# Kernel tuning notes

Measured on AMD Instinct MI355X. Metric: run time of the kernel, lower is better.

## Reference

```python
import jax, jax.numpy as jnp
import numpy as np

B, S, D, H = 2, 2048, 1024, 16
DK = D // H


def layernorm(x, gamma, bias, eps=1e-6):
    m = jnp.mean(x, axis=-1, keepdims=True)
    v = jnp.mean((x - m) ** 2, axis=-1, keepdims=True)  # biased var (correction=0)
    return gamma * (x - m) / jnp.sqrt(v + eps) + bias


def setup_inputs() -> dict:
    key = jax.random.key(0)
    ks = jax.random.split(key, 10)
    xav = (2.0 / (D + D)) ** 0.5  # xavier_normal_ std for square [D,D]
    lin1_b = (1.0 / D) ** 0.5     # nn.Linear default init bound
    lin2_b = (1.0 / (4 * D)) ** 0.5
    return {
        "X": jax.random.normal(ks[0], (B, S, D), jnp.float32),
        "padding_mask": jnp.ones((B, 1, S), jnp.int32),
        "W_Q": jax.random.normal(ks[1], (D, D), jnp.float32) * xav,
        "W_K": jax.random.normal(ks[2], (D, D), jnp.float32) * xav,
        "W_V": jax.random.normal(ks[3], (D, D), jnp.float32) * xav,
        "W_O": jax.random.normal(ks[4], (D, D), jnp.float32) * xav,
        "g1": jnp.ones((D,), jnp.float32),
        "b1": jnp.zeros((D,), jnp.float32),
        "W1": jax.random.uniform(ks[5], (D, 4 * D), jnp.float32, -lin1_b, lin1_b),
        "bias1": jax.random.uniform(ks[6], (4 * D,), jnp.float32, -lin1_b, lin1_b),
        "W2": jax.random.uniform(ks[7], (4 * D, D), jnp.float32, -lin2_b, lin2_b),
        "bias2": jax.random.uniform(ks[8], (D,), jnp.float32, -lin2_b, lin2_b),
        "g2": jnp.ones((D,), jnp.float32),
        "b2": jnp.zeros((D,), jnp.float32),
    }


def reference(X, padding_mask, W_Q, W_K, W_V, W_O, g1, b1, W1, bias1, W2, bias2, g2, b2):
    b, s, d = X.shape
    # pre-norm + MHA
    xn = layernorm(X, g1, b1)
    q = (xn @ W_Q).reshape(b, s, H, DK).transpose(0, 2, 1, 3)  # [B,H,S,DK]
    k = (xn @ W_K).reshape(b, s, H, DK).transpose(0, 2, 1, 3)
    v = (xn @ W_V).reshape(b, s, H, DK).transpose(0, 2, 1, 3)
    scores = jnp.einsum("bhqd,bhkd->bhqk", q, k) / np.sqrt(DK).astype(np.float32)
    mask = padding_mask[:, None, :, :]  # [B,1,1,S] broadcast over heads/queries
    scores = jnp.where(mask == 0, jnp.float32(-1e9), scores)
    w = jax.nn.softmax(scores, axis=-1)
    attn = jnp.einsum("bhqk,bhkd->bhqd", w, v)
    attn = attn.transpose(0, 2, 1, 3).reshape(b, s, d) @ W_O
    out = attn + X
    # pre-norm + GELU FFN (exact erf GELU, matching nn.GELU default)
    nn2 = layernorm(out, g2, b2)
    ff = jax.nn.gelu(nn2 @ W1 + bias1, approximate=False) @ W2 + bias2
    return ff + out
```

## Files before the change

### kernel.cpp

```cpp
#include <hip/hip_runtime.h>
#include <hip/hip_bf16.h>


using bf16 = __hip_bfloat16;
typedef __attribute__((ext_vector_type(4))) float f32x4;
typedef __attribute__((ext_vector_type(16))) float f32x16;
typedef __attribute__((ext_vector_type(8))) short bf16x8;

#define DEVI static __device__ __forceinline__

DEVI void async_copy16(const void* g, void* l) {
  __builtin_amdgcn_global_load_lds(
      (const __attribute__((address_space(1))) void*)g,
      (__attribute__((address_space(3))) void*)l, 16, 0, 0);
}

DEVI ushort f2bf_bits(float v) {
  __hip_bfloat16 h = __float2bfloat16(v);
  return *reinterpret_cast<ushort*>(&h);
}

DEVI float bfbits2f(ushort u) {
  union { float f; unsigned int i; } x;
  x.i = ((unsigned int)u) << 16;
  return x.f;
}

DEVI unsigned int pk2(float lo, float hi) {
  return (unsigned int)f2bf_bits(lo) | ((unsigned int)f2bf_bits(hi) << 16);
}

__global__ __launch_bounds__(256) void ln_kernel(
    const float* __restrict__ in, const float* __restrict__ gamma,
    const float* __restrict__ beta, bf16* __restrict__ out) {
  const long row = blockIdx.x;
  const int t = threadIdx.x;
  float4 x = ((const float4*)(in + row * 1024))[t];
  float s = x.x + x.y + x.z + x.w;
  float s2 = x.x * x.x + x.y * x.y + x.z * x.z + x.w * x.w;
#pragma unroll
  for (int m = 1; m < 64; m <<= 1) {
    s += __shfl_xor(s, m);
    s2 += __shfl_xor(s2, m);
  }
  __shared__ float red[8];
  const int w = t >> 6, l = t & 63;
  if (l == 0) { red[w] = s; red[4 + w] = s2; }
  __syncthreads();
  s = red[0] + red[1] + red[2] + red[3];
  s2 = red[4] + red[5] + red[6] + red[7];
  const float mean = s * (1.0f / 1024.0f);
  const float var = s2 * (1.0f / 1024.0f) - mean * mean;
  const float rstd = rsqrtf(var + 1e-6f);
  float4 g4 = ((const float4*)gamma)[t];
  float4 b4 = ((const float4*)beta)[t];
  union { ushort h[4]; uint2 u; } o;
  o.h[0] = f2bf_bits(g4.x * (x.x - mean) * rstd + b4.x);
  o.h[1] = f2bf_bits(g4.y * (x.y - mean) * rstd + b4.y);
  o.h[2] = f2bf_bits(g4.z * (x.z - mean) * rstd + b4.z);
  o.h[3] = f2bf_bits(g4.w * (x.w - mean) * rstd + b4.w);
  ((uint2*)(out + row * 1024))[t] = o.u;
}

__global__ __launch_bounds__(256) void oproj_reduce_ln(
    const float* __restrict__ p0, const float* __restrict__ p1,
    const float* __restrict__ X, const float* __restrict__ gamma,
    const float* __restrict__ beta, float* __restrict__ res_out,
    bf16* __restrict__ xn_out) {
  const long row = blockIdx.x;
  const int t = threadIdx.x;
  const long i = row * 256 + t;
  const float4 a = ((const float4*)p0)[i];
  const float4 b = ((const float4*)p1)[i];
  const float4 c = ((const float4*)X)[i];
  float4 x;
  x.x = a.x + b.x + c.x; x.y = a.y + b.y + c.y;
  x.z = a.z + b.z + c.z; x.w = a.w + b.w + c.w;
  ((float4*)res_out)[i] = x;
  float s = x.x + x.y + x.z + x.w;
  float s2 = x.x * x.x + x.y * x.y + x.z * x.z + x.w * x.w;
#pragma unroll
  for (int m = 1; m < 64; m <<= 1) {
    s += __shfl_xor(s, m);
    s2 += __shfl_xor(s2, m);
  }
  __shared__ float red[8];
  const int w = t >> 6, l = t & 63;
  if (l == 0) { red[w] = s; red[4 + w] = s2; }
  __syncthreads();
  s = red[0] + red[1] + red[2] + red[3];
  s2 = red[4] + red[5] + red[6] + red[7];
  const float mean = s * (1.0f / 1024.0f);
  const float var = s2 * (1.0f / 1024.0f) - mean * mean;
  const float rstd = rsqrtf(var + 1e-6f);
  float4 g4 = ((const float4*)gamma)[t];
  float4 b4 = ((const float4*)beta)[t];
  union { ushort h[4]; uint2 u; } o;
  o.h[0] = f2bf_bits(g4.x * (x.x - mean) * rstd + b4.x);
  o.h[1] = f2bf_bits(g4.y * (x.y - mean) * rstd + b4.y);
  o.h[2] = f2bf_bits(g4.z * (x.z - mean) * rstd + b4.z);
  o.h[3] = f2bf_bits(g4.w * (x.w - mean) * rstd + b4.w);
  ((uint2*)(xn_out + row * 1024))[t] = o.u;
}

__global__ __launch_bounds__(256) void transpose_all(
    const float* __restrict__ q, const float* __restrict__ k,
    const float* __restrict__ v, const float* __restrict__ o,
    const float* __restrict__ w1, const float* __restrict__ w2,
    bf16* __restrict__ wqkvo, bf16* __restrict__ w1t, bf16* __restrict__ w2t) {
  const int tid = blockIdx.x;
  const float* W;
  bf16* Wt;
  int K, N, n0, k0;
  if (tid < 4096) {
    const int z = tid >> 10, r = tid & 1023;
    W = (z == 0) ? q : (z == 1) ? k : (z == 2) ? v : o;
    Wt = wqkvo + (size_t)z * 1024 * 1024;
    K = 1024; N = 1024; n0 = (r & 31) << 5; k0 = (r >> 5) << 5;
  } else if (tid < 8192) {
    const int r = tid - 4096;
    W = w1; Wt = w1t; K = 1024; N = 4096;
    n0 = (r & 127) << 5; k0 = (r >> 7) << 5;
  } else {
    const int r = tid - 8192;
    W = w2; Wt = w2t; K = 4096; N = 1024;
    n0 = (r & 31) << 5; k0 = (r >> 5) << 5;
  }
  __shared__ float tile[32][33];
  const int tx = threadIdx.x & 31, ty = threadIdx.x >> 5;
#pragma unroll
  for (int i = 0; i < 32; i += 8)
    tile[ty + i][tx] = W[(long)(k0 + ty + i) * N + n0 + tx];
  __syncthreads();
#pragma unroll
  for (int i = 0; i < 32; i += 8)
    Wt[(long)(n0 + ty + i) * K + k0 + tx] = __float2bfloat16(tile[tx][ty + i]);
}

template <int EPI, int KSPLIT>
__global__ __launch_bounds__(256) void gemm_bt(
    const bf16* __restrict__ A, const bf16* __restrict__ Bt,
    const int M, const int N, const int K, const int lda, const int ldb,
    const float* __restrict__ bias, const float* __restrict__ res,
    float* __restrict__ pother, void* __restrict__ Cout) {
  __shared__ bf16 As[128 * 64];
  __shared__ bf16 Bs[128 * 64];
  const int t = threadIdx.x;
  const int w = t >> 6, l = t & 63;
  const int nb = N >> 7;
  const int cpx = gridDim.x >> 3;
  int bidx = (blockIdx.x & 7) * cpx + (blockIdx.x >> 3);
  int sl = 0;
  if (KSPLIT == 2) {
    const int half = gridDim.x >> 1;
    sl = bidx >= half;
    bidx -= sl * half;
  }
  const int bm = bidx / nb, bn = bidx % nb;
  const long row0 = (long)bm << 7, col0 = (long)bn << 7;
  const int wr = (w >> 1) << 6, wc = (w & 1) << 6;
  const int lr = l & 15;
  const int lkb = (l >> 4) << 4;

  f32x4 acc[4][4];
#pragma unroll
  for (int m = 0; m < 4; ++m)
#pragma unroll
    for (int n = 0; n < 4; ++n) acc[m][n] = (f32x4){0.f, 0.f, 0.f, 0.f};

  const int rA = t >> 3;
  const int g = (t & 7) ^ ((t >> 3) & 7);
  const bf16* gA = A + (row0 + rA) * (long)lda + (long)sl * K + g * 8;
  const bf16* gB = Bt + (col0 + rA) * (long)ldb + (long)sl * K + g * 8;
  char* lA = (char*)As + t * 16;
  char* lB = (char*)Bs + t * 16;

  for (int k0 = 0; k0 < K; k0 += 64) {
    __syncthreads();
#pragma unroll
    for (int cr = 0; cr < 4; ++cr) {
      async_copy16(gA + (long)cr * 32 * lda + k0, lA + cr * 4096);
      async_copy16(gB + (long)cr * 32 * ldb + k0, lB + cr * 4096);
    }
    __syncthreads();
#pragma unroll
    for (int ks = 0; ks < 2; ++ks) {
      bf16x8 af[4], bfr[4];
#pragma unroll
      for (int m = 0; m < 4; ++m) {
        const int row = wr + m * 16 + lr;
        af[m] = *(const bf16x8*)((const char*)As +
            (row * 128 + ((ks * 64 + lkb) ^ ((row & 7) << 4))));
      }
#pragma unroll
      for (int n = 0; n < 4; ++n) {
        const int row = wc + n * 16 + lr;
        bfr[n] = *(const bf16x8*)((const char*)Bs +
            (row * 128 + ((ks * 64 + lkb) ^ ((row & 7) << 4))));
      }
#pragma unroll
      for (int m = 0; m < 4; ++m)
#pragma unroll
        for (int n = 0; n < 4; ++n)
          acc[m][n] = __builtin_amdgcn_mfma_f32_16x16x32_bf16(af[m], bfr[n], acc[m][n], 0, 0, 0);
    }
  }

  bf16* Cb = (bf16*)Cout;
  float* Cf = (float*)Cout;
  if ((EPI == 4 || EPI == 5) && sl == 1) Cf = pother;
#pragma unroll
  for (int m = 0; m < 4; ++m) {
#pragma unroll
    for (int r = 0; r < 4; ++r) {
      const long crow = row0 + wr + m * 16 + ((l >> 4) << 2) + r;
      const long rbase = crow * N;
#pragma unroll
      for (int n = 0; n < 4; ++n) {
        const long ccol = col0 + wc + n * 16 + lr;
        float v = acc[m][n][r];
        if (EPI == 2) {
          const float vv = v + bias[ccol];
          const float u2 = vv * (1.5957691216f + 0.0713548162f * vv * vv);
          v = vv / (1.0f + __expf(-u2));
        }
        if (EPI == 5 && sl == 0) v += bias[ccol] + res[rbase + ccol];
        if (EPI == 0 || EPI == 2)
          Cb[rbase + ccol] = __float2bfloat16(v);
        else
          Cf[rbase + ccol] = v;
      }
    }
  }
}

__global__ __launch_bounds__(256) void ff2_reduce(
    const float* __restrict__ p0, const float* __restrict__ p1,
    float* __restrict__ out) {
  const int idx = blockIdx.x * 256 + threadIdx.x;
  const float4 x = ((const float4*)p0)[idx];
  const float4 y = ((const float4*)p1)[idx];
  float4 a;
  a.x = x.x + y.x; a.y = x.y + y.y; a.z = x.z + y.z; a.w = x.w + y.w;
  ((float4*)out)[idx] = a;
}

__global__ __launch_bounds__(512) void attn_kernel(
    const bf16* __restrict__ QKV, const int* __restrict__ pmask,
    bf16* __restrict__ Oout) {
  const int bh = blockIdx.x;
  const int b = bh >> 4, h = bh & 15;
  const int q0 = blockIdx.y << 8;
  const int t = threadIdx.x;
  const int w = t >> 6, l = t & 63;
  const int lq = l & 31, hi = l >> 5;

  __shared__ __align__(16) char smem[65536];

  const long base = (long)b * 2048 * 3072;
  const bf16* Qg = QKV + base + h * 64;
  const bf16* Kg = QKV + base + 1024 + h * 64;
  const bf16* Vg = QKV + base + 2048 + h * 64;

  int kSrc[2], kDst[2], vk[2], vsg[2];
#pragma unroll
  for (int p = 0; p < 2; ++p) {
    const int c = p * 512 + t;
    const int kr = c >> 3;
    kSrc[p] = kr * 3072 + (((c & 7) ^ (kr & 7)) << 3);
    kDst[p] = c * 16;
    vk[p] = c >> 3;
    vsg[p] = c & 7;
  }

  const int qw0 = q0 + w * 32;
  bf16x8 qf[4];
#pragma unroll
  for (int dc = 0; dc < 4; ++dc) {
    uint4 raw = *(const uint4*)(Qg + (long)(qw0 + lq) * 3072 + dc * 16 + hi * 8);
    union { uint4 u4; ushort us[8]; } in; in.u4 = raw;
    union { bf16x8 v; ushort us[8]; } o;
#pragma unroll
    for (int e = 0; e < 8; ++e) o.us[e] = f2bf_bits(0.125f * bfbits2f(in.us[e]));
    qf[dc] = o.v;
  }

  union { unsigned int u[4]; bf16x8 v; } bones;
  bones.u[0] = (hi == 0) ? 0x00003F80u : 0u;
  bones.u[1] = bones.u[2] = bones.u[3] = 0u;

  uint4 vreg[2];
#pragma unroll
  for (int p = 0; p < 2; ++p) {
    vreg[p] = *(const uint4*)(Vg + (long)vk[p] * 3072 + vsg[p] * 8);
    async_copy16(Kg + kSrc[p], smem + kDst[p]);
  }
#pragma unroll
  for (int p = 0; p < 2; ++p) {
    const ushort* vs = (const ushort*)&vreg[p];
#pragma unroll
    for (int e = 0; e < 8; ++e) {
      const int d = vsg[p] * 8 + e;
      *(ushort*)(smem + 32768 + d * 256 +
                 ((vk[p] * 2) ^ (((e ^ vsg[p]) & 7) << 4))) = vs[e];
    }
  }

  f32x16 oacc[2];
#pragma unroll
  for (int nt = 0; nt < 2; ++nt)
#pragma unroll
    for (int r = 0; r < 16; ++r) oacc[nt][r] = 0.f;
  float mrun = -3.0e38f, lsum = 0.f;
  int cur = 0;

  __syncthreads();

  for (int ktg = 0; ktg < 16; ++ktg) {
    if (ktg < 15) {
      const long nrow0 = (long)(ktg + 1) * 128 * 3072;
#pragma unroll
      for (int p = 0; p < 2; ++p) {
        vreg[p] = *(const uint4*)(Vg + nrow0 + (long)vk[p] * 3072 + vsg[p] * 8);
        async_copy16(Kg + nrow0 + kSrc[p], smem + (cur ^ 1) * 16384 + kDst[p]);
      }
    }
    const int k0 = ktg << 7;
    const char* Ks = smem + cur * 16384;
    const char* Vt = smem + 32768 + cur * 16384;

    f32x16 sacc[4];
    __builtin_amdgcn_s_setprio(1);
#pragma unroll
    for (int kt = 0; kt < 4; ++kt) {
#pragma unroll
      for (int r = 0; r < 16; ++r) sacc[kt][r] = 0.f;
#pragma unroll
      for (int dc = 0; dc < 4; ++dc) {
        bf16x8 ka = *(const bf16x8*)(Ks +
            ((kt * 32 + lq) * 128 + ((dc * 32 + hi * 16) ^ ((lq & 7) << 4))));
        sacc[kt] = __builtin_amdgcn_mfma_f32_32x32x16_bf16(ka, qf[dc], sacc[kt], 0, 0, 0);
      }
      const int mv = pmask[b * 2048 + k0 + kt * 32 + lq];
      union { unsigned int u[4]; bf16x8 v; } aadd;
      aadd.u[0] = (hi == 0 && mv == 0) ? (unsigned int)f2bf_bits(-1.0e9f) : 0u;
      aadd.u[1] = aadd.u[2] = aadd.u[3] = 0u;
      sacc[kt] = __builtin_amdgcn_mfma_f32_32x32x16_bf16(aadd.v, bones.v, sacc[kt], 0, 0, 0);
    }
    __builtin_amdgcn_s_setprio(0);

    float tmax = -3.0e38f;
#pragma unroll
    for (int kt = 0; kt < 4; ++kt)
#pragma unroll
      for (int r = 0; r < 16; ++r) tmax = fmaxf(tmax, sacc[kt][r]);
    tmax = fmaxf(tmax, __shfl_xor(tmax, 32));
    const bool need = (bool)__any(tmax > mrun + 8.0f);
    const float mnew = need ? fmaxf(mrun, tmax) : mrun;
    float psum = 0.f;
#pragma unroll
    for (int kt = 0; kt < 4; ++kt)
#pragma unroll
      for (int r = 0; r < 16; ++r) {
        const float p = __expf(sacc[kt][r] - mnew);
        sacc[kt][r] = p;
        psum += p;
      }
    psum += __shfl_xor(psum, 32);
    if (need) {
      const float alpha = __expf(mrun - mnew);
      mrun = mnew;
      lsum = lsum * alpha + psum;
#pragma unroll
      for (int r = 0; r < 16; ++r) {
        const float ar = __shfl(alpha, (r & 3) + 8 * (r >> 2) + 4 * hi);
        oacc[0][r] *= ar;
        oacc[1][r] *= ar;
      }
    } else {
      lsum += psum;
    }

    union { unsigned int u[4]; bf16x8 v; } paE[4], paO[4];
#pragma unroll
    for (int kt = 0; kt < 4; ++kt) {
      const unsigned int cs0 = pk2(sacc[kt][0], sacc[kt][1]);
      const unsigned int cs1 = pk2(sacc[kt][2], sacc[kt][3]);
      const unsigned int cs2 = pk2(sacc[kt][4], sacc[kt][5]);
      const unsigned int cs3 = pk2(sacc[kt][6], sacc[kt][7]);
      const unsigned int cs4 = pk2(sacc[kt][8], sacc[kt][9]);
      const unsigned int cs5 = pk2(sacc[kt][10], sacc[kt][11]);
      const unsigned int cs6 = pk2(sacc[kt][12], sacc[kt][13]);
      const unsigned int cs7 = pk2(sacc[kt][14], sacc[kt][15]);
      const unsigned int es0 = __shfl_xor(cs0, 32);
      const unsigned int es1 = __shfl_xor(cs1, 32);
      const unsigned int es2 = __shfl_xor(cs2, 32);
      const unsigned int es3 = __shfl_xor(cs3, 32);
      const unsigned int es4 = __shfl_xor(cs4, 32);
      const unsigned int es5 = __shfl_xor(cs5, 32);
      const unsigned int es6 = __shfl_xor(cs6, 32);
      const unsigned int es7 = __shfl_xor(cs7, 32);
      paE[kt].u[0] = hi ? es2 : cs0;
      paE[kt].u[1] = hi ? es3 : cs1;
      paE[kt].u[2] = hi ? cs2 : es0;
      paE[kt].u[3] = hi ? cs3 : es1;
      paO[kt].u[0] = hi ? es6 : cs4;
      paO[kt].u[1] = hi ? es7 : cs5;
      paO[kt].u[2] = hi ? cs6 : es4;
      paO[kt].u[3] = hi ? cs7 : es5;
    }

    __builtin_amdgcn_s_setprio(1);
#pragma unroll
    for (int kt = 0; kt < 4; ++kt)
#pragma unroll
      for (int nt = 0; nt < 2; ++nt) {
        const int vrow = nt * 32 + lq;
        const int vsw = ((vrow & 7) ^ ((vrow >> 3) & 7)) << 4;
        bf16x8 vbE = *(const bf16x8*)(Vt + (vrow * 256 + ((kt * 64 + hi * 16) ^ vsw)));
        oacc[nt] = __builtin_amdgcn_mfma_f32_32x32x16_bf16(paE[kt].v, vbE, oacc[nt], 0, 0, 0);
        bf16x8 vbO = *(const bf16x8*)(Vt + (vrow * 256 + ((kt * 64 + 32 + hi * 16) ^ vsw)));
        oacc[nt] = __builtin_amdgcn_mfma_f32_32x32x16_bf16(paO[kt].v, vbO, oacc[nt], 0, 0, 0);
      }
    __builtin_amdgcn_s_setprio(0);

    if (ktg < 15) {
      char* VtN = smem + 32768 + (cur ^ 1) * 16384;
#pragma unroll
      for (int p = 0; p < 2; ++p) {
        const ushort* vs = (const ushort*)&vreg[p];
#pragma unroll
        for (int e = 0; e < 8; ++e) {
          const int d = vsg[p] * 8 + e;
          *(ushort*)(VtN + d * 256 +
                     ((vk[p] * 2) ^ (((e ^ vsg[p]) & 7) << 4))) = vs[e];
        }
      }
    }

    __syncthreads();
    cur ^= 1;
  }

  const float inv = 1.0f / lsum;
#pragma unroll
  for (int r = 0; r < 16; ++r) {
    const int crow = (r & 3) + 8 * (r >> 2) + 4 * hi;
    const float ir = __shfl(inv, crow);
    const long orow = (long)b * 2048 + qw0 + crow;
#pragma unroll
    for (int nt = 0; nt < 2; ++nt)
      Oout[orow * 1024 + h * 64 + nt * 32 + lq] = __float2bfloat16(oacc[nt][r] * ir);
  }
}

extern "C" void kernel_launch(void* const* d_in, const int* in_sizes, int n_in,
                              void* d_out, int out_size, void* d_ws, size_t ws_size,
                              hipStream_t stream) {
  const float* X = (const float*)d_in[0];
  const int* pmask = (const int*)d_in[1];
  const float* W_Q = (const float*)d_in[2];
  const float* W_K = (const float*)d_in[3];
  const float* W_V = (const float*)d_in[4];
  const float* W_O = (const float*)d_in[5];
  const float* g1 = (const float*)d_in[6];
  const float* b1 = (const float*)d_in[7];
  const float* W1 = (const float*)d_in[8];
  const float* bias1 = (const float*)d_in[9];
  const float* W2 = (const float*)d_in[10];
  const float* bias2 = (const float*)d_in[11];
  const float* g2 = (const float*)d_in[12];
  const float* b2 = (const float*)d_in[13];
  (void)in_sizes; (void)n_in; (void)out_size; (void)ws_size;

  char* ws = (char*)d_ws;
  const size_t MB = 1ull << 20;
  bf16* W1_t   = (bf16*)(ws + 0);
  bf16* Wqkv_t = (bf16*)(ws + 8 * MB);
  bf16* Wo_t   = (bf16*)(ws + 14 * MB);
  bf16* W2_t   = (bf16*)(ws + 16 * MB);
  bf16* xn     = (bf16*)(ws + 24 * MB);
  bf16* QKV    = (bf16*)(ws + 32 * MB);
  bf16* attnb  = (bf16*)(ws + 56 * MB);
  bf16* ff1    = (bf16*)(ws + 32 * MB);
  float* p0o   = (float*)(ws + 64 * MB);
  float* p1o   = (float*)(ws + 32 * MB);
  float* p0    = (float*)(ws + 64 * MB);
  float* p1    = (float*)(ws + 0);
  float* res1  = (float*)d_out;

  transpose_all<<<12288, 256, 0, stream>>>(W_Q, W_K, W_V, W_O, W1, W2,
                                           Wqkv_t, W1_t, W2_t);
  ln_kernel<<<4096, 256, 0, stream>>>(X, g1, b1, xn);
  gemm_bt<0, 1><<<32 * 24, 256, 0, stream>>>(xn, Wqkv_t, 4096, 3072, 1024, 1024, 1024,
                                             nullptr, nullptr, nullptr, QKV);
  attn_kernel<<<dim3(32, 8), 512, 0, stream>>>(QKV, pmask, attnb);
  gemm_bt<4, 2><<<2 * 32 * 8, 256, 0, stream>>>(attnb, Wo_t, 4096, 1024, 512, 1024, 1024,
                                                nullptr, nullptr, p1o, p0o);
  oproj_reduce_ln<<<4096, 256, 0, stream>>>(p0o, p1o, X, g2, b2, res1, xn);
  gemm_bt<2, 1><<<32 * 32, 256, 0, stream>>>(xn, W1_t, 4096, 4096, 1024, 1024, 1024,
                                             bias1, nullptr, nullptr, ff1);
  gemm_bt<5, 2><<<2 * 32 * 8, 256, 0, stream>>>(ff1, W2_t, 4096, 1024, 2048, 4096, 4096,
                                                bias2, res1, p1, p0);
  ff2_reduce<<<4096, 256, 0, stream>>>(p0, p1, res1);
}
```

Measured before the change: 287.0 us.

## Double-buffer GEMM shared-memory tiles with async prefetch of next K tile

```diff
diff --git a/kernel.cpp b/kernel.cpp
--- a/kernel.cpp
+++ b/kernel.cpp
@@ -143,8 +143,7 @@
     const int M, const int N, const int K, const int lda, const int ldb,
     const float* __restrict__ bias, const float* __restrict__ res,
     float* __restrict__ pother, void* __restrict__ Cout) {
-  __shared__ bf16 As[128 * 64];
-  __shared__ bf16 Bs[128 * 64];
+  __shared__ __align__(16) char gsmem[65536];
   const int t = threadIdx.x;
   const int w = t >> 6, l = t & 63;
   const int nb = N >> 7;
@@ -172,30 +171,45 @@
   const int g = (t & 7) ^ ((t >> 3) & 7);
   const bf16* gA = A + (row0 + rA) * (long)lda + (long)sl * K + g * 8;
   const bf16* gB = Bt + (col0 + rA) * (long)ldb + (long)sl * K + g * 8;
-  char* lA = (char*)As + t * 16;
-  char* lB = (char*)Bs + t * 16;
-
-  for (int k0 = 0; k0 < K; k0 += 64) {
-    __syncthreads();
-#pragma unroll
-    for (int cr = 0; cr < 4; ++cr) {
-      async_copy16(gA + (long)cr * 32 * lda + k0, lA + cr * 4096);
-      async_copy16(gB + (long)cr * 32 * ldb + k0, lB + cr * 4096);
-    }
-    __syncthreads();
+
+  const int nt = K >> 6;
+#pragma unroll
+  for (int cr = 0; cr < 4; ++cr) {
+    async_copy16(gA + (long)cr * 32 * lda, gsmem + t * 16 + cr * 4096);
+    async_copy16(gB + (long)cr * 32 * ldb, gsmem + 16384 + t * 16 + cr * 4096);
+  }
+  int cur = 0;
+
+  for (int kt = 0; kt < nt; ++kt) {
+    if (kt < nt - 1) {
+      const int k1 = (kt + 1) << 6;
+      char* dst = gsmem + (cur ^ 1) * 32768;
+#pragma unroll
+      for (int cr = 0; cr < 4; ++cr) {
+        async_copy16(gA + (long)cr * 32 * lda + k1, dst + t * 16 + cr * 4096);
+        async_copy16(gB + (long)cr * 32 * ldb + k1, dst + 16384 + t * 16 + cr * 4096);
+      }
+      asm volatile("s_waitcnt vmcnt(8)" ::: "memory");
+    } else {
+      asm volatile("s_waitcnt vmcnt(0)" ::: "memory");
+    }
+    __builtin_amdgcn_s_barrier();
+    __builtin_amdgcn_sched_barrier(0);
+    const char* As = gsmem + cur * 32768;
+    const char* Bs = As + 16384;
 #pragma unroll
     for (int ks = 0; ks < 2; ++ks) {
       bf16x8 af[4], bfr[4];
 #pragma unroll
       for (int m = 0; m < 4; ++m) {
         const int row = wr + m * 16 + lr;
-        af[m] = *(const bf16x8*)((const char*)As +
+        af[m] = *(const bf16x8*)(As +
             (row * 128 + ((ks * 64 + lkb) ^ ((row & 7) << 4))));
       }
 #pragma unroll
       for (int n = 0; n < 4; ++n) {
         const int row = wc + n * 16 + lr;
-        bfr[n] = *(const bf16x8*)((const char*)Bs +
+        bfr[n] = *(const bf16x8*)(Bs +
             (row * 128 + ((ks * 64 + lkb) ^ ((row & 7) << 4))));
       }
 #pragma unroll
@@ -204,6 +218,9 @@
         for (int n = 0; n < 4; ++n)
           acc[m][n] = __builtin_amdgcn_mfma_f32_16x16x32_bf16(af[m], bfr[n], acc[m][n], 0, 0, 0);
     }
+    __builtin_amdgcn_sched_barrier(0);
+    __builtin_amdgcn_s_barrier();
+    cur ^= 1;
   }
 
   bf16* Cb = (bf16*)Cout;
```

Measured after the change: 267.6 us. -6.8%, faster.
